# Optimization experiments

Measured on AMD Instinct MI355X. Metric: run time of the kernel, lower is better.

## Reference

```python
import jax, jax.numpy as jnp
import numpy as np
from math import factorial

IRREPS_IN1 = [(128, 0), (64, 1), (32, 2)]  # (mul, l): features
IRREPS_IN2 = [(1, 0), (1, 1), (1, 2)]      # spherical harmonics lmax=2
BATCH = 16384

# ---------- real Clebsch-Gordan coefficients (e3nn convention) ----------

def _su2_cg(j1, j2, j3, m1, m2, m3):
    if m3 != m1 + m2:
        return 0.0
    f = factorial
    pref = ((2 * j3 + 1) * f(j1 + j2 - j3) * f(j1 - j2 + j3) * f(-j1 + j2 + j3) / f(j1 + j2 + j3 + 1)) ** 0.5
    pref *= (f(j3 + m3) * f(j3 - m3) * f(j1 - m1) * f(j1 + m1) * f(j2 - m2) * f(j2 + m2)) ** 0.5
    s = 0.0
    for v in range(0, j1 + j2 - j3 + 1):
        a = j1 + j2 - j3 - v; b = j1 - m1 - v; c = j2 + m2 - v
        d = j3 - j2 + m1 + v; e = j3 - j1 - m2 + v
        if min(a, b, c, d, e) < 0:
            continue
        s += (-1) ** v / (f(v) * f(a) * f(b) * f(c) * f(d) * f(e))
    return pref * s


def _su2_cg_tensor(l1, l2, l3):
    C = np.zeros((2 * l1 + 1, 2 * l2 + 1, 2 * l3 + 1))
    for m1 in range(-l1, l1 + 1):
        for m2 in range(-l2, l2 + 1):
            for m3 in range(-l3, l3 + 1):
                C[l1 + m1, l2 + m2, l3 + m3] = _su2_cg(l1, l2, l3, m1, m2, m3)
    return C


def _q(l):
    # change of basis real -> complex spherical harmonics
    q = np.zeros((2 * l + 1, 2 * l + 1), dtype=np.complex128)
    for m in range(-l, 0):
        q[l + m, l + abs(m)] = 1.0 / np.sqrt(2.0)
        q[l + m, l - abs(m)] = -1j / np.sqrt(2.0)
    q[l, l] = 1.0
    for m in range(1, l + 1):
        q[l + m, l + abs(m)] = (-1) ** m / np.sqrt(2.0)
        q[l + m, l - abs(m)] = 1j * (-1) ** m / np.sqrt(2.0)
    return (-1j) ** l * q


def _real_cg(l1, l2, l3):
    C = _su2_cg_tensor(l1, l2, l3).astype(np.complex128)
    Q1, Q2, Q3 = _q(l1), _q(l2), _q(l3)
    C = np.einsum('ij,kl,mn,ikn->jlm', Q1, Q2, np.conj(Q3.T), C)
    assert np.abs(C.imag).max() < 1e-8
    return np.ascontiguousarray(C.real.astype(np.float32))

# precompute all CG tensors needed by the full tensor product
CG = {}
for _m1, _l1 in IRREPS_IN1:
    for _m2, _l2 in IRREPS_IN2:
        for _l3 in range(abs(_l1 - _l2), _l1 + _l2 + 1):
            if (_l1, _l2, _l3) not in CG:
                CG[(_l1, _l2, _l3)] = _real_cg(_l1, _l2, _l3)


def _tensor_product(x, y):
    """Full CG tensor product. x:[B,480] y:[B,9] -> dict l3 -> list of [B,mul,2l3+1]."""
    B = x.shape[0]
    outs = {}
    off1 = 0
    for mul1, l1 in IRREPS_IN1:
        d1 = 2 * l1 + 1
        x_blk = x[:, off1:off1 + mul1 * d1].reshape(B, mul1, d1)
        off1 += mul1 * d1
        off2 = 0
        for mul2, l2 in IRREPS_IN2:
            d2 = 2 * l2 + 1
            y_blk = y[:, off2:off2 + mul2 * d2].reshape(B, mul2, d2)
            off2 += mul2 * d2
            for l3 in range(abs(l1 - l2), l1 + l2 + 1):
                cg = jnp.asarray(CG[(l1, l2, l3)])  # [d1,d2,d3]
                z = jnp.einsum('ijk,bui,bvj->buvk', cg, x_blk, y_blk)
                outs.setdefault(l3, []).append(z.reshape(B, mul1 * mul2, 2 * l3 + 1))
    return outs


def setup_inputs() -> dict:
    key = jax.random.key(0)
    k = jax.random.split(key, 5)
    dim1 = sum(m * (2 * l + 1) for m, l in IRREPS_IN1)  # 480
    dim2 = sum(m * (2 * l + 1) for m, l in IRREPS_IN2)  # 9
    x = jax.random.normal(k[0], (BATCH, dim1), dtype=jnp.float32)
    y = jax.random.normal(k[1], (BATCH, dim2), dtype=jnp.float32)
    # fan-in per output l of the equivariant Linear (tp outputs with matching l)
    W0 = jax.random.normal(k[2], (224, 128), dtype=jnp.float32)
    W1 = jax.random.normal(k[3], (384, 64), dtype=jnp.float32)
    W2 = jax.random.normal(k[4], (352, 32), dtype=jnp.float32)
    return {"x": x, "y": y, "W0": W0, "W1": W1, "W2": W2}


def reference(x, y, W0, W1, W2):
    B = x.shape[0]
    outs = _tensor_product(x, y)
    Ws = {0: W0, 1: W1, 2: W2}
    res = []
    for mul_out, l in IRREPS_IN1:
        blk = jnp.concatenate(outs[l], axis=1)  # [B, tot_mul, 2l+1]
        tot_mul = blk.shape[1]
        o = jnp.einsum('bui,uv->bvi', blk, Ws[l]) / np.sqrt(tot_mul).astype(np.float32)
        res.append(o.reshape(B, mul_out * (2 * l + 1)))
    return jnp.concatenate(res, axis=1)  # [B, 480]
```

## Files before the change

### kernel.cpp

```cpp
#include <hip/hip_runtime.h>
#include <math.h>
#include <stdint.h>

#define NBATCH 16384
#define MB 16
#define NT 256
#define NBLOCKS (NBATCH/MB)
#define WT_BYTE_OFF 2560
#define XPITCH 488

typedef float  f32x4 __attribute__((ext_vector_type(4)));
typedef short  s16x8 __attribute__((ext_vector_type(8)));

__device__ const int P_CGOFF[15] = {0,1,10,35,44,53,80,125,170,245,270,315,390,415,490};
__device__ const int P_D2[15]    = {1,3,5,3,1,3,5,3,5,5,3,5,1,3,5};
__device__ const int P_D3[15]    = {1,1,1,3,3,3,3,3,3,5,5,5,5,5,5};
__device__ const int P_TSTART[15]= {0,1,4,9,12,21,30,39,54,69,74,89,104,129,154};
__device__ const int P_YOFF[15]  = {0,1,4,1,0,1,4,1,4,4,1,4,0,1,4};
__device__ const int CG_L1[15] = {0,1,2,0,1,1,1,2,2,0,1,1,2,2,2};
__device__ const int CG_L2[15] = {0,1,2,1,0,1,2,1,2,2,1,2,0,1,2};
__device__ const int CG_L3[15] = {0,0,0,1,1,1,1,1,1,2,2,2,2,2,2};

__device__ const int   SEG_WB[15] = {0,16384,24576, 28672,36864,40960,45056,49152,51200,
                                     53248,57344,59392,61440,62464,63488};
__device__ const int   SEG_SH[15] = {7,6,5, 7,6,6,6,5,5, 7,6,6,5,5,5};
__device__ const int   SEG_U0[15] = {0,128,192, 0,128,192,256,320,352, 0,128,192,256,288,320};
__device__ const int   SEG_G[15]  = {0,0,0, 1,1,1,1,1,1, 2,2,2,2,2,2};
__device__ const float SEG_SC[3]  = {0.066815310478f, 0.051031036308f, 0.053300179089f};

__device__ const float FCT[13] = {1.f,1.f,2.f,6.f,24.f,120.f,720.f,5040.f,40320.f,
                                  362880.f,3628800.f,39916800.f,479001600.f};

__device__ float su2f(int j1,int j2,int j3,int m1,int m2,int m3){
  float pref = sqrtf((float)(2*j3+1)*FCT[j1+j2-j3]*FCT[j1-j2+j3]*FCT[-j1+j2+j3]/FCT[j1+j2+j3+1]);
  pref *= sqrtf(FCT[j3+m3]*FCT[j3-m3]*FCT[j1-m1]*FCT[j1+m1]*FCT[j2-m2]*FCT[j2+m2]);
  float s = 0.f;
  for (int v=0; v<=j1+j2-j3; ++v){
    int a=j1+j2-j3-v, b=j1-m1-v, c=j2+m2-v, d=j3-j2+m1+v, e=j3-j1-m2+v;
    if (a<0||b<0||c<0||d<0||e<0) continue;
    float term = 1.f/(FCT[v]*FCT[a]*FCT[b]*FCT[c]*FCT[d]*FCT[e]);
    s += (v&1) ? -term : term;
  }
  return pref*s;
}

__device__ void qvalf(int l,int r,int c,float* qr,float* qi){
  int m = r - l;
  const float is2 = 0.70710678118654752440f;
  float br=0.f, bi=0.f;
  if (m<0){
    if (c == l - m) br = is2;
    else if (c == l + m) bi = -is2;
  } else if (m==0){
    if (c==l) br = 1.f;
  } else {
    float sg = (m&1)? -1.f : 1.f;
    if (c == l + m) br = sg*is2;
    else if (c == l - m) bi = sg*is2;
  }
  if (l==1){ float nr = bi, ni = -br; br=nr; bi=ni; }
  else if (l==2){ br=-br; bi=-bi; }
  *qr=br; *qi=bi;
}

__device__ __forceinline__ uint32_t f2bf(float f){
  uint32_t u = __float_as_uint(f);
  return (u + 0x7fffu + ((u>>16)&1u)) >> 16;
}
__device__ __forceinline__ float bf2f(uint32_t v){ return __uint_as_float(v << 16); }

__global__ void prep(const float* __restrict__ W0, const float* __restrict__ W1,
                     const float* __restrict__ W2, float* __restrict__ ws)
{
  int t = blockIdx.x*NT + threadIdx.x;
  if (t < 64512){
    uint16_t* wt = (uint16_t*)((char*)ws + WT_BYTE_OFF);
    int j = 0;
    while (j < 14 && t >= SEG_WB[j+1]) ++j;
    int idx = t - SEG_WB[j];
    int sh = SEG_SH[j];
    int v  = idx >> sh, u1 = idx & ((1<<sh)-1);
    int g  = SEG_G[j];
    int N  = (g==0)?128:(g==1)?64:32;
    const float* Wsrc = (g==0)?W0:(g==1)?W1:W2;
    wt[t] = (uint16_t)f2bf(Wsrc[(SEG_U0[j]+u1)*N + v] * SEG_SC[g]);
  }
  int t2 = t - 64512;
  if (t2 >= 0 && t2 < 615*25){
    int e = t2/25, ik = t2 - e*25;
    int i = ik/5, k = ik - (ik/5)*5;
    int p = 0;
    while (p < 14 && e >= P_CGOFF[p+1]) ++p;
    int r = e - P_CGOFF[p];
    int d2 = P_D2[p], d3 = P_D3[p];
    int i1 = r/(d2*d3); int rem = r - i1*(d2*d3);
    int i2 = rem/d3;    int i3 = rem - i2*d3;
    int l1 = CG_L1[p], l2 = CG_L2[p], l3 = CG_L3[p];
    if (i <= 2*l1 && k <= 2*l2){
      int n = i + k - l1 - l2 + l3;
      if (n >= 0 && n <= 2*l3){
        float c = su2f(l1,l2,l3, i-l1, k-l2, n-l3);
        if (c != 0.f){
          float q1r,q1i,q2r,q2i,q3r,q3i;
          qvalf(l1,i,i1,&q1r,&q1i);
          qvalf(l2,k,i2,&q2r,&q2i);
          qvalf(l3,n,i3,&q3r,&q3i);
          q3i = -q3i;
          float ar = q1r*q2r - q1i*q2i;
          float ai = q1r*q2i + q1i*q2r;
          float contrib = (ar*q3r - ai*q3i)*c;
          if (contrib != 0.f) atomicAdd(&ws[e], contrib);
        }
      }
    }
  }
}

template<int G> struct GM;
template<> struct GM<0>{
  static constexpr int NS=3, D3=1, OB=0, NMT=2, NI3=1;
  static constexpr int MUL[3]={128,64,32};
  static constexpr int D1[3] ={1,3,5};
  static constexpr int XB[3] ={0,128,320};
  static constexpr int TS[3] ={0,1,4};
  static constexpr int WB[3] ={0,16384,24576};
};
template<> struct GM<1>{
  static constexpr int NS=6, D3=3, OB=128, NMT=1, NI3=3;
  static constexpr int MUL[6]={128,64,64,64,32,32};
  static constexpr int D1[6] ={1,3,3,3,5,5};
  static constexpr int XB[6] ={0,128,128,128,320,320};
  static constexpr int TS[6] ={9,12,21,30,39,54};
  static constexpr int WB[6] ={28672,36864,40960,45056,49152,51200};
};
template<> struct GM<2>{
  static constexpr int NS=6, D3=5, OB=320, NMT=1, NI3=3;
  static constexpr int MUL[6]={128,64,64,32,32,32};
  static constexpr int D1[6] ={1,3,3,5,5,5};
  static constexpr int XB[6] ={0,128,128,320,320,320};
  static constexpr int TS[6] ={69,74,89,104,129,154};
  static constexpr int WB[6] ={53248,57344,59392,61440,62464,63488};
};

template<int G, int S, int NMT, int NI3>
__device__ __forceinline__ void do_seg(const short* __restrict__ wt,
                                       const uint16_t* __restrict__ xp,
                                       const uint16_t* __restrict__ Tsh,
                                       f32x4 (&acc)[NMT][NI3],
                                       int ln, int koct, int mt0, int i3base, int ni3)
{
  using M = GM<G>;
  constexpr int MUL = M::MUL[S];
  constexpr int KS  = MUL >> 5;
  constexpr int D1  = M::D1[S];

  s16x8 Af[NMT][KS];
  #pragma unroll
  for (int mt = 0; mt < NMT; ++mt)
    #pragma unroll
    for (int kk = 0; kk < KS; ++kk)
      Af[mt][kk] = *(const s16x8*)(wt + M::WB[S] + ((mt0+mt)*16 + ln)*MUL + kk*32 + koct);

  #pragma unroll
  for (int i1 = 0; i1 < D1; ++i1){
    s16x8 Bf[KS];
    #pragma unroll
    for (int kk = 0; kk < KS; ++kk)
      Bf[kk] = *(const s16x8*)((const short*)xp + ln*XPITCH + M::XB[S] + i1*MUL + kk*32 + koct);
    #pragma unroll
    for (int mt = 0; mt < NMT; ++mt){
      f32x4 D = {0.f,0.f,0.f,0.f};
      #pragma unroll
      for (int kk = 0; kk < KS; ++kk)
        D = __builtin_amdgcn_mfma_f32_16x16x32_bf16(Af[mt][kk], Bf[kk], D, 0, 0, 0);
      #pragma unroll
      for (int j = 0; j < NI3; ++j){
        if (j < ni3){
          const int e = M::TS[S] + i1*M::D3 + i3base + j;
          const float tv = bf2f(Tsh[e*16 + ln]);
          acc[mt][j][0] += tv*D[0];
          acc[mt][j][1] += tv*D[1];
          acc[mt][j][2] += tv*D[2];
          acc[mt][j][3] += tv*D[3];
        }
      }
    }
  }
}

template<int G>
__device__ __forceinline__ void run_group(const short* __restrict__ wt,
                                          float* __restrict__ out, int b0, int tid,
                                          const uint16_t* __restrict__ Tsh,
                                          const uint16_t* __restrict__ xp)
{
  using M = GM<G>;
  const int lane = tid & 63, w = tid >> 6;
  const int ln   = lane & 15;
  const int koct = (lane >> 4) * 8;
  constexpr int NMT = M::NMT, NI3 = M::NI3;

  int mt0, i3base, ni3;
  if constexpr (G == 0){ mt0 = 2*w; i3base = 0; ni3 = 1; }
  else if constexpr (G == 1){ mt0 = w; i3base = 0; ni3 = 3; }
  else { mt0 = w >> 1; i3base = (w & 1)*3; ni3 = (w & 1) ? 2 : 3; }

  f32x4 acc[NMT][NI3];
  #pragma unroll
  for (int a = 0; a < NMT; ++a)
    #pragma unroll
    for (int b = 0; b < NI3; ++b) acc[a][b] = (f32x4){0.f,0.f,0.f,0.f};

  do_seg<G,0,NMT,NI3>(wt, xp, Tsh, acc, ln, koct, mt0, i3base, ni3);
  do_seg<G,1,NMT,NI3>(wt, xp, Tsh, acc, ln, koct, mt0, i3base, ni3);
  do_seg<G,2,NMT,NI3>(wt, xp, Tsh, acc, ln, koct, mt0, i3base, ni3);
  if constexpr (M::NS > 3){
    do_seg<G,(M::NS>3)?3:0,NMT,NI3>(wt, xp, Tsh, acc, ln, koct, mt0, i3base, ni3);
    do_seg<G,(M::NS>4)?4:0,NMT,NI3>(wt, xp, Tsh, acc, ln, koct, mt0, i3base, ni3);
    do_seg<G,(M::NS>5)?5:0,NMT,NI3>(wt, xp, Tsh, acc, ln, koct, mt0, i3base, ni3);
  }

  const int rq = (lane >> 4) * 4;
  float* orow = out + (size_t)(b0 + ln)*480;
  if constexpr (G == 0){
    #pragma unroll
    for (int mt = 0; mt < NMT; ++mt){
      const int vb = (mt0+mt)*16 + rq;
      float4 st = make_float4(acc[mt][0][0], acc[mt][0][1], acc[mt][0][2], acc[mt][0][3]);
      *(float4*)(orow + vb) = st;
    }
  } else if constexpr (G == 1){
    const int vb = mt0*16 + rq;
    float buf[12];
    #pragma unroll
    for (int r = 0; r < 4; ++r)
      #pragma unroll
      for (int j = 0; j < 3; ++j) buf[r*3+j] = acc[0][j][r];
    float* p = orow + 128 + vb*3;
    *(float4*)(p)   = make_float4(buf[0],buf[1],buf[2],buf[3]);
    *(float4*)(p+4) = make_float4(buf[4],buf[5],buf[6],buf[7]);
    *(float4*)(p+8) = make_float4(buf[8],buf[9],buf[10],buf[11]);
  } else {
    const int vb = mt0*16 + rq;
    #pragma unroll
    for (int r = 0; r < 4; ++r)
      #pragma unroll
      for (int j = 0; j < 3; ++j)
        if (j < ni3)
          orow[320 + (vb+r)*5 + i3base + j] = acc[0][j][r];
  }
}

__device__ __forceinline__ int xmap(int c){
  if (c < 128) return c;
  if (c < 320){ int t = c - 128; int u = t/3; int i1 = t - u*3; return 128 + i1*64 + u; }
  int t = c - 320; int u = t/5; int i1 = t - u*5; return 320 + i1*32 + u;
}

__global__ __launch_bounds__(NT) void tp_linear(
    const float* __restrict__ x, const float* __restrict__ y,
    const float* __restrict__ ws, float* __restrict__ out)
{
  __shared__ __align__(16) uint16_t xp[MB*XPITCH];
  __shared__ __align__(16) uint16_t Tsh[179*16];
  __shared__ __align__(16) float    cgs[616];
  __shared__ __align__(16) float    ysm[MB*12];

  const int tid = threadIdx.x;
  const int b0 = blockIdx.x * MB;
  const short* wt = (const short*)((const char*)ws + WT_BYTE_OFF);

  for (int i = tid; i < 615; i += NT) cgs[i] = ws[i];
  for (int i = tid; i < MB*9; i += NT){
    int b = i/9, c = i - b*9;
    ysm[b*12 + c] = y[(size_t)b0*9 + i];
  }
  for (int i = tid; i < MB*120; i += NT){
    int b = i/120, q = i - b*120;
    float4 v = ((const float4*)(x + (size_t)(b0+b)*480))[q];
    int c = q*4;
    xp[b*XPITCH + xmap(c)]   = (uint16_t)f2bf(v.x);
    xp[b*XPITCH + xmap(c+1)] = (uint16_t)f2bf(v.y);
    xp[b*XPITCH + xmap(c+2)] = (uint16_t)f2bf(v.z);
    xp[b*XPITCH + xmap(c+3)] = (uint16_t)f2bf(v.w);
  }
  __syncthreads();

  for (int i = tid; i < 179*16; i += NT){
    const int e = i >> 4, b = i & 15;
    int p = 0;
    while (p < 14 && e >= P_TSTART[p+1]) ++p;
    const int r = e - P_TSTART[p];
    const int d3 = P_D3[p], d2 = P_D2[p];
    const int i1 = r / d3, j3 = r - (r/d3)*d3;
    const float* cgp = cgs + P_CGOFF[p] + (i1*d2)*d3 + j3;
    const float* yp  = ysm + b*12 + P_YOFF[p];
    float t = 0.f;
    for (int i2 = 0; i2 < d2; ++i2) t += cgp[i2*d3]*yp[i2];
    Tsh[e*16 + b] = (uint16_t)f2bf(t);
  }
  __syncthreads();

  run_group<0>(wt, out, b0, tid, Tsh, xp);
  run_group<1>(wt, out, b0, tid, Tsh, xp);
  run_group<2>(wt, out, b0, tid, Tsh, xp);
}

extern "C" void kernel_launch(void* const* d_in, const int* in_sizes, int n_in,
                              void* d_out, int out_size, void* d_ws, size_t ws_size,
                              hipStream_t stream)
{
  const float* x  = (const float*)d_in[0];
  const float* y  = (const float*)d_in[1];
  const float* W0 = (const float*)d_in[2];
  const float* W1 = (const float*)d_in[3];
  const float* W2 = (const float*)d_in[4];
  float* out = (float*)d_out;
  float* ws  = (float*)d_ws;

  hipMemsetAsync(d_ws, 0, 2464, stream);
  hipLaunchKernelGGL(prep, dim3(313), dim3(NT), 0, stream, W0, W1, W2, ws);
  hipLaunchKernelGGL(tp_linear, dim3(NBLOCKS), dim3(NT), 0, stream, x, y, ws, out);
}
```

Before: 136.7 us.

## Vectorize x staging with packed bf16 stores and a transposed copy, drop memset

```diff
diff --git a/kernel.cpp b/kernel.cpp
--- a/kernel.cpp
+++ b/kernel.cpp
@@ -7,7 +7,8 @@
 #define NT 256
 #define NBLOCKS (NBATCH/MB)
 #define WT_BYTE_OFF 2560
-#define XPITCH 488
+#define XRP 488
+#define XQP 360
 
 typedef float  f32x4 __attribute__((ext_vector_type(4)));
 typedef short  s16x8 __attribute__((ext_vector_type(8)));
@@ -20,13 +21,6 @@
 __device__ const int CG_L1[15] = {0,1,2,0,1,1,1,2,2,0,1,1,2,2,2};
 __device__ const int CG_L2[15] = {0,1,2,1,0,1,2,1,2,2,1,2,0,1,2};
 __device__ const int CG_L3[15] = {0,0,0,1,1,1,1,1,1,2,2,2,2,2,2};
-
-__device__ const int   SEG_WB[15] = {0,16384,24576, 28672,36864,40960,45056,49152,51200,
-                                     53248,57344,59392,61440,62464,63488};
-__device__ const int   SEG_SH[15] = {7,6,5, 7,6,6,6,5,5, 7,6,6,5,5,5};
-__device__ const int   SEG_U0[15] = {0,128,192, 0,128,192,256,320,352, 0,128,192,256,288,320};
-__device__ const int   SEG_G[15]  = {0,0,0, 1,1,1,1,1,1, 2,2,2,2,2,2};
-__device__ const float SEG_SC[3]  = {0.066815310478f, 0.051031036308f, 0.053300179089f};
 
 __device__ const float FCT[13] = {1.f,1.f,2.f,6.f,24.f,120.f,720.f,5040.f,40320.f,
                                   362880.f,3628800.f,39916800.f,479001600.f};
@@ -68,27 +62,32 @@
   return (u + 0x7fffu + ((u>>16)&1u)) >> 16;
 }
 __device__ __forceinline__ float bf2f(uint32_t v){ return __uint_as_float(v << 16); }
+__device__ __forceinline__ uint32_t pk2(float a, float b){ return (f2bf(b)<<16) | f2bf(a); }
 
 __global__ void prep(const float* __restrict__ W0, const float* __restrict__ W1,
                      const float* __restrict__ W2, float* __restrict__ ws)
 {
-  int t = blockIdx.x*NT + threadIdx.x;
-  if (t < 64512){
-    uint16_t* wt = (uint16_t*)((char*)ws + WT_BYTE_OFF);
-    int j = 0;
-    while (j < 14 && t >= SEG_WB[j+1]) ++j;
-    int idx = t - SEG_WB[j];
-    int sh = SEG_SH[j];
-    int v  = idx >> sh, u1 = idx & ((1<<sh)-1);
-    int g  = SEG_G[j];
-    int N  = (g==0)?128:(g==1)?64:32;
-    const float* Wsrc = (g==0)?W0:(g==1)?W1:W2;
-    wt[t] = (uint16_t)f2bf(Wsrc[(SEG_U0[j]+u1)*N + v] * SEG_SC[g]);
-  }
-  int t2 = t - 64512;
-  if (t2 >= 0 && t2 < 615*25){
-    int e = t2/25, ik = t2 - e*25;
-    int i = ik/5, k = ik - (ik/5)*5;
+  const int t = blockIdx.x*NT + threadIdx.x;
+  uint16_t* wt = (uint16_t*)((char*)ws + WT_BYTE_OFF);
+  if (t < 28672){
+    int u = t>>7, v = t&127, wb, mul, u1;
+    if (u<128){wb=0; mul=128; u1=u;} else if (u<192){wb=16384; mul=64; u1=u-128;}
+    else {wb=24576; mul=32; u1=u-192;}
+    wt[wb + v*mul + u1] = (uint16_t)f2bf(W0[t]*0.066815310478f);
+  } else if (t < 53248){
+    int t2 = t-28672, u = t2>>6, v = t2&63, wb, mul, u1;
+    if (u<128){wb=28672; mul=128; u1=u;} else if (u<192){wb=36864; mul=64; u1=u-128;}
+    else if (u<256){wb=40960; mul=64; u1=u-192;} else if (u<320){wb=45056; mul=64; u1=u-256;}
+    else if (u<352){wb=49152; mul=32; u1=u-320;} else {wb=51200; mul=32; u1=u-352;}
+    wt[wb + v*mul + u1] = (uint16_t)f2bf(W1[t2]*0.051031036308f);
+  } else if (t < 64512){
+    int t3 = t-53248, u = t3>>5, v = t3&31, wb, mul, u1;
+    if (u<128){wb=53248; mul=128; u1=u;} else if (u<192){wb=57344; mul=64; u1=u-128;}
+    else if (u<256){wb=59392; mul=64; u1=u-192;} else if (u<288){wb=61440; mul=32; u1=u-256;}
+    else if (u<320){wb=62464; mul=32; u1=u-288;} else {wb=63488; mul=32; u1=u-320;}
+    wt[wb + v*mul + u1] = (uint16_t)f2bf(W2[t3]*0.053300179089f);
+  } else if (t < 64512 + 615){
+    const int e = t - 64512;
     int p = 0;
     while (p < 14 && e >= P_CGOFF[p+1]) ++p;
     int r = e - P_CGOFF[p];
@@ -96,23 +95,24 @@
     int i1 = r/(d2*d3); int rem = r - i1*(d2*d3);
     int i2 = rem/d3;    int i3 = rem - i2*d3;
     int l1 = CG_L1[p], l2 = CG_L2[p], l3 = CG_L3[p];
-    if (i <= 2*l1 && k <= 2*l2){
-      int n = i + k - l1 - l2 + l3;
-      if (n >= 0 && n <= 2*l3){
+    float acc = 0.f;
+    for (int i = 0; i <= 2*l1; ++i){
+      for (int k = 0; k <= 2*l2; ++k){
+        int n = i + k - l1 - l2 + l3;
+        if (n < 0 || n > 2*l3) continue;
         float c = su2f(l1,l2,l3, i-l1, k-l2, n-l3);
-        if (c != 0.f){
-          float q1r,q1i,q2r,q2i,q3r,q3i;
-          qvalf(l1,i,i1,&q1r,&q1i);
-          qvalf(l2,k,i2,&q2r,&q2i);
-          qvalf(l3,n,i3,&q3r,&q3i);
-          q3i = -q3i;
-          float ar = q1r*q2r - q1i*q2i;
-          float ai = q1r*q2i + q1i*q2r;
-          float contrib = (ar*q3r - ai*q3i)*c;
-          if (contrib != 0.f) atomicAdd(&ws[e], contrib);
-        }
+        if (c == 0.f) continue;
+        float q1r,q1i,q2r,q2i,q3r,q3i;
+        qvalf(l1,i,i1,&q1r,&q1i);
+        qvalf(l2,k,i2,&q2r,&q2i);
+        qvalf(l3,n,i3,&q3r,&q3i);
+        q3i = -q3i;
+        float ar = q1r*q2r - q1i*q2i;
+        float ai = q1r*q2i + q1i*q2r;
+        acc += (ar*q3r - ai*q3i)*c;
       }
     }
+    ws[e] = acc;
   }
 }
 
@@ -121,7 +121,8 @@
   static constexpr int NS=3, D3=1, OB=0, NMT=2, NI3=1;
   static constexpr int MUL[3]={128,64,32};
   static constexpr int D1[3] ={1,3,5};
-  static constexpr int XB[3] ={0,128,320};
+  static constexpr bool RAW[3]={true,false,false};
+  static constexpr int PB[3] ={0,0,192};
   static constexpr int TS[3] ={0,1,4};
   static constexpr int WB[3] ={0,16384,24576};
 };
@@ -129,7 +130,8 @@
   static constexpr int NS=6, D3=3, OB=128, NMT=1, NI3=3;
   static constexpr int MUL[6]={128,64,64,64,32,32};
   static constexpr int D1[6] ={1,3,3,3,5,5};
-  static constexpr int XB[6] ={0,128,128,128,320,320};
+  static constexpr bool RAW[6]={true,false,false,false,false,false};
+  static constexpr int PB[6] ={0,0,0,0,192,192};
   static constexpr int TS[6] ={9,12,21,30,39,54};
   static constexpr int WB[6] ={28672,36864,40960,45056,49152,51200};
 };
@@ -137,14 +139,16 @@
   static constexpr int NS=6, D3=5, OB=320, NMT=1, NI3=3;
   static constexpr int MUL[6]={128,64,64,32,32,32};
   static constexpr int D1[6] ={1,3,3,5,5,5};
-  static constexpr int XB[6] ={0,128,128,320,320,320};
+  static constexpr bool RAW[6]={true,false,false,false,false,false};
+  static constexpr int PB[6] ={0,0,0,192,192,192};
   static constexpr int TS[6] ={69,74,89,104,129,154};
   static constexpr int WB[6] ={53248,57344,59392,61440,62464,63488};
 };
 
 template<int G, int S, int NMT, int NI3>
 __device__ __forceinline__ void do_seg(const short* __restrict__ wt,
-                                       const uint16_t* __restrict__ xp,
+                                       const uint16_t* __restrict__ xr,
+                                       const uint16_t* __restrict__ xq,
                                        const uint16_t* __restrict__ Tsh,
                                        f32x4 (&acc)[NMT][NI3],
                                        int ln, int koct, int mt0, int i3base, int ni3)
@@ -161,12 +165,19 @@
     for (int kk = 0; kk < KS; ++kk)
       Af[mt][kk] = *(const s16x8*)(wt + M::WB[S] + ((mt0+mt)*16 + ln)*MUL + kk*32 + koct);
 
+  const short* xbase = M::RAW[S] ? ((const short*)xr + ln*XRP)
+                                 : ((const short*)xq + ln*XQP + M::PB[S]);
   #pragma unroll
   for (int i1 = 0; i1 < D1; ++i1){
+    float tv[NI3];
+    #pragma unroll
+    for (int j = 0; j < NI3; ++j)
+      if (j < ni3)
+        tv[j] = bf2f(Tsh[(M::TS[S] + i1*M::D3 + i3base + j)*16 + ln]);
     s16x8 Bf[KS];
     #pragma unroll
     for (int kk = 0; kk < KS; ++kk)
-      Bf[kk] = *(const s16x8*)((const short*)xp + ln*XPITCH + M::XB[S] + i1*MUL + kk*32 + koct);
+      Bf[kk] = *(const s16x8*)(xbase + i1*MUL + kk*32 + koct);
     #pragma unroll
     for (int mt = 0; mt < NMT; ++mt){
       f32x4 D = {0.f,0.f,0.f,0.f};
@@ -176,12 +187,10 @@
       #pragma unroll
       for (int j = 0; j < NI3; ++j){
         if (j < ni3){
-          const int e = M::TS[S] + i1*M::D3 + i3base + j;
-          const float tv = bf2f(Tsh[e*16 + ln]);
-          acc[mt][j][0] += tv*D[0];
-          acc[mt][j][1] += tv*D[1];
-          acc[mt][j][2] += tv*D[2];
-          acc[mt][j][3] += tv*D[3];
+          acc[mt][j][0] += tv[j]*D[0];
+          acc[mt][j][1] += tv[j]*D[1];
+          acc[mt][j][2] += tv[j]*D[2];
+          acc[mt][j][3] += tv[j]*D[3];
         }
       }
     }
@@ -192,7 +201,8 @@
 __device__ __forceinline__ void run_group(const short* __restrict__ wt,
                                           float* __restrict__ out, int b0, int tid,
                                           const uint16_t* __restrict__ Tsh,
-                                          const uint16_t* __restrict__ xp)
+                                          const uint16_t* __restrict__ xr,
+                                          const uint16_t* __restrict__ xq)
 {
   using M = GM<G>;
   const int lane = tid & 63, w = tid >> 6;
@@ -211,13 +221,13 @@
     #pragma unroll
     for (int b = 0; b < NI3; ++b) acc[a][b] = (f32x4){0.f,0.f,0.f,0.f};
 
-  do_seg<G,0,NMT,NI3>(wt, xp, Tsh, acc, ln, koct, mt0, i3base, ni3);
-  do_seg<G,1,NMT,NI3>(wt, xp, Tsh, acc, ln, koct, mt0, i3base, ni3);
-  do_seg<G,2,NMT,NI3>(wt, xp, Tsh, acc, ln, koct, mt0, i3base, ni3);
+  do_seg<G,0,NMT,NI3>(wt, xr, xq, Tsh, acc, ln, koct, mt0, i3base, ni3);
+  do_seg<G,1,NMT,NI3>(wt, xr, xq, Tsh, acc, ln, koct, mt0, i3base, ni3);
+  do_seg<G,2,NMT,NI3>(wt, xr, xq, Tsh, acc, ln, koct, mt0, i3base, ni3);
   if constexpr (M::NS > 3){
-    do_seg<G,(M::NS>3)?3:0,NMT,NI3>(wt, xp, Tsh, acc, ln, koct, mt0, i3base, ni3);
-    do_seg<G,(M::NS>4)?4:0,NMT,NI3>(wt, xp, Tsh, acc, ln, koct, mt0, i3base, ni3);
-    do_seg<G,(M::NS>5)?5:0,NMT,NI3>(wt, xp, Tsh, acc, ln, koct, mt0, i3base, ni3);
+    do_seg<G,(M::NS>3)?3:0,NMT,NI3>(wt, xr, xq, Tsh, acc, ln, koct, mt0, i3base, ni3);
+    do_seg<G,(M::NS>4)?4:0,NMT,NI3>(wt, xr, xq, Tsh, acc, ln, koct, mt0, i3base, ni3);
+    do_seg<G,(M::NS>5)?5:0,NMT,NI3>(wt, xr, xq, Tsh, acc, ln, koct, mt0, i3base, ni3);
   }
 
   const int rq = (lane >> 4) * 4;
@@ -226,8 +236,8 @@
     #pragma unroll
     for (int mt = 0; mt < NMT; ++mt){
       const int vb = (mt0+mt)*16 + rq;
-      float4 st = make_float4(acc[mt][0][0], acc[mt][0][1], acc[mt][0][2], acc[mt][0][3]);
-      *(float4*)(orow + vb) = st;
+      *(float4*)(orow + vb) = make_float4(acc[mt][0][0], acc[mt][0][1],
+                                          acc[mt][0][2], acc[mt][0][3]);
     }
   } else if constexpr (G == 1){
     const int vb = mt0*16 + rq;
@@ -251,59 +261,74 @@
   }
 }
 
-__device__ __forceinline__ int xmap(int c){
-  if (c < 128) return c;
-  if (c < 320){ int t = c - 128; int u = t/3; int i1 = t - u*3; return 128 + i1*64 + u; }
-  int t = c - 320; int u = t/5; int i1 = t - u*5; return 320 + i1*32 + u;
-}
-
 __global__ __launch_bounds__(NT) void tp_linear(
     const float* __restrict__ x, const float* __restrict__ y,
     const float* __restrict__ ws, float* __restrict__ out)
 {
-  __shared__ __align__(16) uint16_t xp[MB*XPITCH];
+  __shared__ __align__(16) uint16_t xr[MB*XRP];
+  __shared__ __align__(16) uint16_t xq[MB*XQP];
   __shared__ __align__(16) uint16_t Tsh[179*16];
   __shared__ __align__(16) float    cgs[616];
   __shared__ __align__(16) float    ysm[MB*12];
+  __shared__ __align__(16) uint32_t metas[180];
 
   const int tid = threadIdx.x;
   const int b0 = blockIdx.x * MB;
   const short* wt = (const short*)((const char*)ws + WT_BYTE_OFF);
 
+  if (tid < MB*9){
+    int b = tid/9, c = tid - b*9;
+    ysm[b*12 + c] = y[(size_t)b0*9 + tid];
+  }
   for (int i = tid; i < 615; i += NT) cgs[i] = ws[i];
-  for (int i = tid; i < MB*9; i += NT){
-    int b = i/9, c = i - b*9;
-    ysm[b*12 + c] = y[(size_t)b0*9 + i];
-  }
-  for (int i = tid; i < MB*120; i += NT){
-    int b = i/120, q = i - b*120;
-    float4 v = ((const float4*)(x + (size_t)(b0+b)*480))[q];
-    int c = q*4;
-    xp[b*XPITCH + xmap(c)]   = (uint16_t)f2bf(v.x);
-    xp[b*XPITCH + xmap(c+1)] = (uint16_t)f2bf(v.y);
-    xp[b*XPITCH + xmap(c+2)] = (uint16_t)f2bf(v.z);
-    xp[b*XPITCH + xmap(c+3)] = (uint16_t)f2bf(v.w);
-  }
-  __syncthreads();
-
-  for (int i = tid; i < 179*16; i += NT){
-    const int e = i >> 4, b = i & 15;
+  for (int e = tid; e < 179; e += NT){
     int p = 0;
     while (p < 14 && e >= P_TSTART[p+1]) ++p;
     const int r = e - P_TSTART[p];
     const int d3 = P_D3[p], d2 = P_D2[p];
     const int i1 = r / d3, j3 = r - (r/d3)*d3;
-    const float* cgp = cgs + P_CGOFF[p] + (i1*d2)*d3 + j3;
-    const float* yp  = ysm + b*12 + P_YOFF[p];
-    float t = 0.f;
-    for (int i2 = 0; i2 < d2; ++i2) t += cgp[i2*d3]*yp[i2];
+    const uint32_t cgi = P_CGOFF[p] + (i1*d2)*d3 + j3;
+    metas[e] = cgi | (d3<<10) | (d2<<13) | (P_YOFF[p]<<16);
+  }
+  for (int idx = tid; idx < MB*120; idx += NT){
+    int b = idx/120, q = idx - b*120;
+    float4 v = ((const float4*)(x + (size_t)(b0+b)*480))[q];
+    *(uint2*)&xr[b*XRP + q*4] = make_uint2(pk2(v.x,v.y), pk2(v.z,v.w));
+  }
+  __syncthreads();
+
+  for (int idx = tid; idx < 1536; idx += NT){
+    const int b = idx/96, rem = idx - b*96;
+    const int i1 = rem >> 5, up = rem & 31;
+    const int s0 = b*XRP + 128 + up*6 + i1;
+    const uint32_t a = xr[s0], c = xr[s0+3];
+    *(uint32_t*)&xq[b*XQP + i1*64 + up*2] = a | (c<<16);
+  }
+  for (int idx = tid; idx < 1280; idx += NT){
+    const int b = idx/80, rem = idx - b*80;
+    const int i1 = rem >> 4, up = rem & 15;
+    const int s0 = b*XRP + 320 + up*10 + i1;
+    const uint32_t a = xr[s0], c = xr[s0+5];
+    *(uint32_t*)&xq[b*XQP + 192 + i1*32 + up*2] = a | (c<<16);
+  }
+  for (int idx = tid; idx < 179*16; idx += NT){
+    const int e = idx >> 4, b = idx & 15;
+    const uint32_t m = metas[e];
+    const int cgi = m & 1023, d3 = (m>>10)&7, d2 = (m>>13)&7, yo = m>>16;
+    const float* cp = cgs + cgi;
+    const float* yp = ysm + b*12 + yo;
+    float t = cp[0]*yp[0];
+    if (d2 > 1){
+      t += cp[d3]*yp[1] + cp[2*d3]*yp[2];
+      if (d2 > 3) t += cp[3*d3]*yp[3] + cp[4*d3]*yp[4];
+    }
     Tsh[e*16 + b] = (uint16_t)f2bf(t);
   }
   __syncthreads();
 
-  run_group<0>(wt, out, b0, tid, Tsh, xp);
-  run_group<1>(wt, out, b0, tid, Tsh, xp);
-  run_group<2>(wt, out, b0, tid, Tsh, xp);
+  run_group<0>(wt, out, b0, tid, Tsh, xr, xq);
+  run_group<1>(wt, out, b0, tid, Tsh, xr, xq);
+  run_group<2>(wt, out, b0, tid, Tsh, xr, xq);
 }
 
 extern "C" void kernel_launch(void* const* d_in, const int* in_sizes, int n_in,
@@ -318,7 +343,6 @@
   float* out = (float*)d_out;
   float* ws  = (float*)d_ws;
 
-  hipMemsetAsync(d_ws, 0, 2464, stream);
-  hipLaunchKernelGGL(prep, dim3(313), dim3(NT), 0, stream, W0, W1, W2, ws);
+  hipLaunchKernelGGL(prep, dim3(255), dim3(NT), 0, stream, W0, W1, W2, ws);
   hipLaunchKernelGGL(tp_linear, dim3(NBLOCKS), dim3(NT), 0, stream, x, y, ws, out);
 }
```

New measurement: 161.5 us. +18.1%, slower.
